# Kernel optimization log

Measured on AMD Instinct MI355X. Metric: run time of the kernel, lower is better.

## Reference

```python
import jax, jax.numpy as jnp
import numpy as np

E = 64        # num_experts
K = 6         # num_experts_per_tok
D = 2048      # hidden_size
F = 1408      # moe_intermediate_size (per expert)
NSH = 2       # num_shared_experts
FS = F * NSH  # shared-expert intermediate
T = 2048      # tokens (batch*seq flattened)
CAP = 512     # expert capacity; mean load T*K/E=192, CAP is >20 sigma above -> no drops


def setup_inputs() -> dict:
    key = jax.random.key(0)
    ks = jax.random.split(key, 9)
    s = 0.02
    return {
        "hidden_states": jax.random.normal(ks[0], (T, D), jnp.float32),
        "gate_w": jax.random.normal(ks[1], (E, D), jnp.float32) * s,
        "w_gate": jax.random.normal(ks[2], (E, D, F), jnp.float32) * s,
        "w_up": jax.random.normal(ks[3], (E, D, F), jnp.float32) * s,
        "w_down": jax.random.normal(ks[4], (E, F, D), jnp.float32) * s,
        "ws_gate": jax.random.normal(ks[5], (D, FS), jnp.float32) * s,
        "ws_up": jax.random.normal(ks[6], (D, FS), jnp.float32) * s,
        "ws_down": jax.random.normal(ks[7], (FS, D), jnp.float32) * s,
    }


def reference(hidden_states, gate_w, w_gate, w_up, w_down, ws_gate, ws_up, ws_down):
    x = hidden_states  # [T, D]
    n_tok = x.shape[0]

    # ---- gate: softmax -> top-k -> renormalize (bailing_moe norm_topk_prob) ----
    probs = jax.nn.softmax(x @ gate_w.T, axis=-1)           # [T, E]
    topw, topi = jax.lax.top_k(probs, K)                    # [T, K]
    topw = topw / jnp.sum(topw, axis=-1, keepdims=True)

    flat_e = topi.reshape(-1)                               # [T*K] expert id per assignment
    flat_w = topw.reshape(-1)                               # [T*K] combine weight
    tok = jnp.arange(n_tok * K) // K                        # [T*K] source token (idxs // k)

    # ---- dispatch: slot of each assignment within its expert (== sort-by-expert) ----
    onehot = jax.nn.one_hot(flat_e, E, dtype=jnp.int32)     # [T*K, E]
    slot = jnp.take_along_axis(jnp.cumsum(onehot, axis=0) - onehot,
                               flat_e[:, None], axis=1)[:, 0]  # [T*K]
    valid = slot < CAP                                      # all True given CAP margin
    slot_c = jnp.where(valid, slot, CAP - 1)

    xa = x[tok] * valid[:, None].astype(x.dtype)            # [T*K, D] gathered tokens
    buf = jnp.zeros((E, CAP, D), x.dtype).at[flat_e, slot_c].add(xa)  # [E, CAP, D]

    # ---- per-expert SwiGLU MLP as grouped GEMMs ----
    h = jax.nn.silu(jnp.einsum('ecd,edf->ecf', buf, w_gate)) \
        * jnp.einsum('ecd,edf->ecf', buf, w_up)             # [E, CAP, F]
    o = jnp.einsum('ecf,efd->ecd', h, w_down)               # [E, CAP, D]

    # ---- combine: weighted scatter-add back to tokens ----
    ya = o[flat_e, slot_c] * (flat_w * valid.astype(flat_w.dtype))[:, None]
    y = jax.ops.segment_sum(ya, tok, num_segments=n_tok)    # [T, D]

    # ---- shared experts (SwiGLU on identity) ----
    shared = (jax.nn.silu(x @ ws_gate) * (x @ ws_up)) @ ws_down
    return y + shared
```

## Files before the change

### kernel.cpp

```cpp
#include <hip/hip_runtime.h>
#include <hip/hip_bf16.h>
#include <cstdint>

typedef __attribute__((ext_vector_type(4))) float f4;
typedef __attribute__((ext_vector_type(4))) float f32x4;
typedef __attribute__((ext_vector_type(8))) __bf16 bf16x8;
typedef unsigned short ushort_t;
typedef unsigned int uint_t;

#define TTOK 2048
#define DDIM 2048
#define NEXP 64
#define TOPK 6
#define FDIM 1408
#define FSH  2816
#define NASSIGN (TTOK*TOPK)

__device__ __forceinline__ ushort_t f2bf(float f){
  uint_t u = __builtin_bit_cast(uint_t, f);
  u = (u + 0x7FFFu + ((u >> 16) & 1u)) >> 16;
  return (ushort_t)u;
}
__device__ __forceinline__ float bf2f(uint_t b){
  uint_t u = (b & 0xFFFFu) << 16;
  return __builtin_bit_cast(float, u);
}
__device__ __forceinline__ void gld_lds16(const void* g, void* l){
  __builtin_amdgcn_global_load_lds((const __attribute__((address_space(1))) uint_t*)g,
                                   (__attribute__((address_space(3))) uint_t*)l, 16, 0, 0);
}

__global__ __launch_bounds__(256) void gate_topk_kernel(
    const float* __restrict__ x, const float* __restrict__ gw,
    int* __restrict__ topi, float* __restrict__ topw)
{
  __shared__ float xs[4*2048];
  __shared__ float lg[4*64];
  int tid = threadIdx.x;
  int t0 = blockIdx.x*4;
  const f4* xg = (const f4*)(x + (size_t)t0*DDIM);
  f4* xsv = (f4*)xs;
  for (int i = tid; i < 2048; i += 256) xsv[i] = xg[i];
  __syncthreads();
  int g = tid >> 6, l = tid & 63;
  int c = l & 3, er = l >> 2;
  const f4* xrow = (const f4*)(xs + g*2048 + c*512);
  #pragma unroll
  for (int eo = 0; eo < 4; ++eo){
    int e = eo*16 + er;
    const f4* wrow = (const f4*)(gw + (size_t)e*DDIM + c*512);
    float d = 0.f;
    #pragma unroll 4
    for (int j = 0; j < 128; ++j){
      f4 w = wrow[j], a = xrow[j];
      d += w.x*a.x + w.y*a.y + w.z*a.z + w.w*a.w;
    }
    d += __shfl_xor(d, 1);
    d += __shfl_xor(d, 2);
    if (c == 0) lg[g*64 + e] = d;
  }
  __syncthreads();
  float mv = lg[g*64 + l];
  float sv[6]; int si[6];
  #pragma unroll
  for (int s = 0; s < 6; ++s){
    float bv = mv; int bi = l;
    for (int off = 32; off > 0; off >>= 1){
      float ov = __shfl_xor(bv, off);
      int oi = __shfl_xor(bi, off);
      if (ov > bv || (ov == bv && oi < bi)){ bv = ov; bi = oi; }
    }
    sv[s] = bv; si[s] = bi;
    if (l == bi) mv = -3.4e38f;
  }
  if (l == 0){
    float sum = 0.f, wv[6];
    #pragma unroll
    for (int s = 0; s < 6; ++s){ wv[s] = __expf(sv[s] - sv[0]); sum += wv[s]; }
    float inv = 1.f/sum;
    int t = t0 + g;
    #pragma unroll
    for (int s = 0; s < 6; ++s){ topi[t*6+s] = si[s]; topw[t*6+s] = wv[s]*inv; }
  }
}

__global__ __launch_bounds__(256) void xcast_kernel(const float* __restrict__ x, ushort_t* __restrict__ xb){
  size_t base = ((size_t)blockIdx.x*256 + threadIdx.x)*8;
  f4 a = *(const f4*)(x + base);
  f4 b = *(const f4*)(x + base + 4);
  uint4 r;
  r.x = f2bf(a.x) | ((uint_t)f2bf(a.y)<<16);
  r.y = f2bf(a.z) | ((uint_t)f2bf(a.w)<<16);
  r.z = f2bf(b.x) | ((uint_t)f2bf(b.y)<<16);
  r.w = f2bf(b.z) | ((uint_t)f2bf(b.w)<<16);
  *(uint4*)(xb + base) = r;
}

__global__ __launch_bounds__(256) void count_kernel(const int* __restrict__ topi, int* __restrict__ counts){
  int a = blockIdx.x*256 + threadIdx.x;
  if (a < NASSIGN) atomicAdd(&counts[topi[a]], 1);
}
__global__ void scan_kernel(const int* __restrict__ counts, int* __restrict__ offsets){
  if (threadIdx.x == 0){
    int s = 0;
    for (int e = 0; e < NEXP; ++e){ offsets[e] = s; s += counts[e]; }
    offsets[NEXP] = s;
  }
}
__global__ __launch_bounds__(256) void scatter_kernel(
    const int* __restrict__ topi, const float* __restrict__ topw,
    const int* __restrict__ offsets, int* __restrict__ cursor,
    int* __restrict__ row_token, float* __restrict__ row_w, int* __restrict__ row_assign)
{
  int a = blockIdx.x*256 + threadIdx.x;
  if (a < NASSIGN){
    int e = topi[a];
    int pos = atomicAdd(&cursor[e], 1);
    int r = offsets[e] + pos;
    row_token[r]  = a / 6;
    row_w[r]      = topw[a];
    row_assign[r] = a;
  }
}

__global__ __launch_bounds__(512, 2) void gemm_gateup_kernel(
    const ushort_t* __restrict__ A, const float* __restrict__ Bg0, const float* __restrict__ Bu0,
    ushort_t* __restrict__ H,
    const int* __restrict__ offsets, const int* __restrict__ row_token,
    const ushort_t* __restrict__ zerop,
    int N, int K, int lda, int n_mt, int n_nt, int Mfix)
{
  int nwg = gridDim.x;
  int chunk = nwg >> 3;
  int L = (blockIdx.x & 7)*chunk + (blockIdx.x >> 3);
  int e, mt, nt, row0, rowcnt;
  if (offsets){
    int per = n_mt*n_nt; e = L/per; int rem = L - e*per; mt = rem/n_nt; nt = rem - mt*n_nt;
    row0 = offsets[e]; rowcnt = offsets[e+1] - row0;
  } else { e = 0; nt = L/n_mt; mt = L - nt*n_mt; row0 = 0; rowcnt = Mfix; }
  int m0 = mt*256;
  if (m0 >= rowcnt) return;

  const float* Bg = Bg0 + (size_t)e*K*N + nt*64;
  const float* Bu = Bu0 + (size_t)e*K*N + nt*64;

  __shared__ ushort_t As[2][256*64];
  __shared__ ushort_t Bs[2][2*64*64];

  int tid = threadIdx.x;
  int lane = tid & 63;
  int wid = tid >> 6;
  int wm = wid & 3, wn = wid >> 2;

  const ushort_t* asrc[4];
  #pragma unroll
  for (int i = 0; i < 4; ++i){
    int r = (tid >> 3) + i*64;
    int gr = m0 + r;
    bool v = gr < rowcnt;
    int tok = row_token ? (v ? row_token[row0+gr] : 0) : gr;
    const ushort_t* p = v ? (A + (size_t)tok*lda) : zerop;
    int slot = (tid & 7) ^ (r & 7);
    asrc[i] = p + slot*8;
  }

  int half = tid >> 8;
  int l256 = tid & 255;
  int bn4 = l256 & 15, bk4 = l256 >> 4;
  const float* Bsrc = half ? Bu : Bg;
  int bdoff[4];
  #pragma unroll
  for (int j = 0; j < 4; ++j){
    int n = bn4*4 + j;
    int slot = (bk4 >> 1) ^ (n & 7);
    bdoff[j] = half*4096 + n*64 + slot*8 + (bk4 & 1)*4;
  }

  f32x4 accG[4][2], accU[4][2];
  #pragma unroll
  for (int i=0;i<4;++i)
    #pragma unroll
    for (int j=0;j<2;++j){ accG[i][j] = f32x4{0.f,0.f,0.f,0.f}; accU[i][j] = f32x4{0.f,0.f,0.f,0.f}; }

  int nK = K >> 6;
  #pragma unroll
  for (int i = 0; i < 4; ++i)
    gld_lds16(asrc[i], &As[0][i*4096 + tid*8]);
  {
    const float* bp = Bsrc + (size_t)(bk4*4)*N + bn4*4;
    f4 v0 = *(const f4*)(bp);
    f4 v1 = *(const f4*)(bp + (size_t)N);
    f4 v2 = *(const f4*)(bp + 2*(size_t)N);
    f4 v3 = *(const f4*)(bp + 3*(size_t)N);
    #pragma unroll
    for (int j = 0; j < 4; ++j){
      uint2 pk;
      pk.x = f2bf(v0[j]) | ((uint_t)f2bf(v1[j]) << 16);
      pk.y = f2bf(v2[j]) | ((uint_t)f2bf(v3[j]) << 16);
      *(uint2*)&Bs[0][bdoff[j]] = pk;
    }
  }
  __syncthreads();

  for (int ks = 0; ks < nK; ++ks){
    int cur = ks & 1, nxt = cur ^ 1;
    bool pf = (ks + 1) < nK;
    if (pf){
      int k0n = (ks + 1) << 6;
      #pragma unroll
      for (int i = 0; i < 4; ++i)
        gld_lds16(asrc[i] + k0n, &As[nxt][i*4096 + tid*8]);
    }
    f4 v0, v1, v2, v3;
    if (pf){
      const float* bp = Bsrc + (size_t)(((ks + 1) << 6) + bk4*4)*N + bn4*4;
      v0 = *(const f4*)(bp);
      v1 = *(const f4*)(bp + (size_t)N);
      v2 = *(const f4*)(bp + 2*(size_t)N);
      v3 = *(const f4*)(bp + 3*(size_t)N);
    }
    #pragma unroll
    for (int kk = 0; kk < 2; ++kk){
      bf16x8 af[4], bg[2], bu[2];
      int kb = (kk << 2) + (lane >> 4);
      #pragma unroll
      for (int i = 0; i < 4; ++i){
        int ar = wm*64 + i*16 + (lane & 15);
        af[i] = *(const bf16x8*)&As[cur][ar*64 + ((kb ^ (ar & 7)) << 3)];
      }
      #pragma unroll
      for (int j = 0; j < 2; ++j){
        int br = wn*32 + j*16 + (lane & 15);
        int idx = br*64 + ((kb ^ (br & 7)) << 3);
        bg[j] = *(const bf16x8*)&Bs[cur][idx];
        bu[j] = *(const bf16x8*)&Bs[cur][4096 + idx];
      }
      #pragma unroll
      for (int i = 0; i < 4; ++i)
        #pragma unroll
        for (int j = 0; j < 2; ++j){
          accG[i][j] = __builtin_amdgcn_mfma_f32_16x16x32_bf16(af[i], bg[j], accG[i][j], 0,0,0);
          accU[i][j] = __builtin_amdgcn_mfma_f32_16x16x32_bf16(af[i], bu[j], accU[i][j], 0,0,0);
        }
    }
    if (pf){
      #pragma unroll
      for (int j = 0; j < 4; ++j){
        uint2 pk;
        pk.x = f2bf(v0[j]) | ((uint_t)f2bf(v1[j]) << 16);
        pk.y = f2bf(v2[j]) | ((uint_t)f2bf(v3[j]) << 16);
        *(uint2*)&Bs[nxt][bdoff[j]] = pk;
      }
    }
    __syncthreads();
  }

  #pragma unroll
  for (int i = 0; i < 4; ++i)
    #pragma unroll
    for (int j = 0; j < 2; ++j){
      int col = nt*64 + wn*32 + j*16 + (lane & 15);
      #pragma unroll
      for (int q = 0; q < 4; ++q){
        int r = wm*64 + i*16 + ((lane >> 4) << 2) + q;
        int gr = m0 + r;
        if (gr < rowcnt){
          float gv = accG[i][j][q];
          float uv = accU[i][j][q];
          float hv = (gv / (1.f + __expf(-gv))) * uv;
          H[(size_t)(row0 + gr)*(size_t)N + col] = f2bf(hv);
        }
      }
    }
}

__global__ __launch_bounds__(512, 4) void gemm_down_kernel(
    const ushort_t* __restrict__ A, const float* __restrict__ B0,
    ushort_t* __restrict__ outb, float* __restrict__ outf,
    const int* __restrict__ offsets, const float* __restrict__ row_w, const int* __restrict__ row_assign,
    const ushort_t* __restrict__ zerop,
    int N, int K, int lda, int n_mt, int n_nt, int Mfix)
{
  int nwg = gridDim.x;
  int chunk = nwg >> 3;
  int L = (blockIdx.x & 7)*chunk + (blockIdx.x >> 3);
  int e, mt, nt, row0, rowcnt;
  if (offsets){
    int per = n_mt*n_nt; e = L/per; int rem = L - e*per; mt = rem/n_nt; nt = rem - mt*n_nt;
    row0 = offsets[e]; rowcnt = offsets[e+1] - row0;
  } else { e = 0; nt = L/n_mt; mt = L - nt*n_mt; row0 = 0; rowcnt = Mfix; }
  int m0 = mt*256;
  if (m0 >= rowcnt) return;

  const float* B = B0 + (size_t)e*K*N + nt*64;

  __shared__ ushort_t As[2][256*64];
  __shared__ ushort_t Bs[2][64*64];
  __shared__ float Wr[256];
  __shared__ int Ar[256];

  int tid = threadIdx.x;
  int lane = tid & 63;
  int wid = tid >> 6;
  int wm = wid & 3, wn = wid >> 2;

  if (offsets){
    for (int t = tid; t < 256; t += 512){
      int gr = m0 + t;
      bool v = gr < rowcnt;
      Wr[t] = v ? row_w[row0+gr] : 0.f;
      Ar[t] = v ? row_assign[row0+gr] : 0;
    }
  }

  const ushort_t* asrc[4];
  #pragma unroll
  for (int i = 0; i < 4; ++i){
    int r = (tid >> 3) + i*64;
    int gr = m0 + r;
    bool v = gr < rowcnt;
    const ushort_t* p = v ? (A + (size_t)(row0+gr)*lda) : zerop;
    int slot = (tid & 7) ^ (r & 7);
    asrc[i] = p + slot*8;
  }

  int bn4 = tid & 15, bk8 = tid >> 4;
  int bdoff[4];
  #pragma unroll
  for (int j = 0; j < 4; ++j){
    int n = bn4*4 + j;
    int slot = (bk8 >> 2) ^ (n & 7);
    bdoff[j] = n*64 + slot*8 + (bk8 & 3)*2;
  }

  f32x4 acc[4][2];
  #pragma unroll
  for (int i=0;i<4;++i)
    #pragma unroll
    for (int j=0;j<2;++j) acc[i][j] = f32x4{0.f,0.f,0.f,0.f};

  int nK = K >> 6;
  #pragma unroll
  for (int i = 0; i < 4; ++i)
    gld_lds16(asrc[i], &As[0][i*4096 + tid*8]);
  {
    const float* bp = B + (size_t)(bk8*2)*N + bn4*4;
    f4 v0 = *(const f4*)(bp);
    f4 v1 = *(const f4*)(bp + (size_t)N);
    #pragma unroll
    for (int j = 0; j < 4; ++j){
      uint_t pk = f2bf(v0[j]) | ((uint_t)f2bf(v1[j]) << 16);
      *(uint_t*)&Bs[0][bdoff[j]] = pk;
    }
  }
  __syncthreads();

  for (int ks = 0; ks < nK; ++ks){
    int cur = ks & 1, nxt = cur ^ 1;
    bool pf = (ks + 1) < nK;
    if (pf){
      int k0n = (ks + 1) << 6;
      #pragma unroll
      for (int i = 0; i < 4; ++i)
        gld_lds16(asrc[i] + k0n, &As[nxt][i*4096 + tid*8]);
    }
    f4 v0, v1;
    if (pf){
      const float* bp = B + (size_t)(((ks + 1) << 6) + bk8*2)*N + bn4*4;
      v0 = *(const f4*)(bp);
      v1 = *(const f4*)(bp + (size_t)N);
    }
    #pragma unroll
    for (int kk = 0; kk < 2; ++kk){
      bf16x8 af[4], bb[2];
      int kb = (kk << 2) + (lane >> 4);
      #pragma unroll
      for (int i = 0; i < 4; ++i){
        int ar = wm*64 + i*16 + (lane & 15);
        af[i] = *(const bf16x8*)&As[cur][ar*64 + ((kb ^ (ar & 7)) << 3)];
      }
      #pragma unroll
      for (int j = 0; j < 2; ++j){
        int br = wn*32 + j*16 + (lane & 15);
        bb[j] = *(const bf16x8*)&Bs[cur][br*64 + ((kb ^ (br & 7)) << 3)];
      }
      #pragma unroll
      for (int i = 0; i < 4; ++i)
        #pragma unroll
        for (int j = 0; j < 2; ++j)
          acc[i][j] = __builtin_amdgcn_mfma_f32_16x16x32_bf16(af[i], bb[j], acc[i][j], 0,0,0);
    }
    if (pf){
      #pragma unroll
      for (int j = 0; j < 4; ++j){
        uint_t pk = f2bf(v0[j]) | ((uint_t)f2bf(v1[j]) << 16);
        *(uint_t*)&Bs[nxt][bdoff[j]] = pk;
      }
    }
    __syncthreads();
  }

  #pragma unroll
  for (int i = 0; i < 4; ++i)
    #pragma unroll
    for (int j = 0; j < 2; ++j){
      int col = nt*64 + wn*32 + j*16 + (lane & 15);
      #pragma unroll
      for (int q = 0; q < 4; ++q){
        int r = wm*64 + i*16 + ((lane >> 4) << 2) + q;
        int gr = m0 + r;
        if (gr < rowcnt){
          float val = acc[i][j][q];
          if (offsets){
            outb[(size_t)Ar[r]*2048 + col] = f2bf(val * Wr[r]);
          } else {
            outf[(size_t)gr*2048 + col] = val;
          }
        }
      }
    }
}

__global__ __launch_bounds__(256) void combine_kernel(const ushort_t* __restrict__ oa, float* __restrict__ out){
  size_t base = ((size_t)blockIdx.x*256 + threadIdx.x)*8;
  int t = (int)(base >> 11);
  int d = (int)(base & 2047);
  f4 s0 = *(const f4*)(out + base);
  f4 s1 = *(const f4*)(out + base + 4);
  #pragma unroll
  for (int k = 0; k < 6; ++k){
    const ushort_t* row = oa + (((size_t)(t*6+k)) << 11) + d;
    uint4 u = *(const uint4*)row;
    s0.x += bf2f(u.x); s0.y += bf2f(u.x >> 16);
    s0.z += bf2f(u.y); s0.w += bf2f(u.y >> 16);
    s1.x += bf2f(u.z); s1.y += bf2f(u.z >> 16);
    s1.z += bf2f(u.w); s1.w += bf2f(u.w >> 16);
  }
  *(f4*)(out + base) = s0;
  *(f4*)(out + base + 4) = s1;
}

extern "C" void kernel_launch(void* const* d_in, const int* in_sizes, int n_in,
                              void* d_out, int out_size, void* d_ws, size_t ws_size,
                              hipStream_t stream)
{
  const float* x       = (const float*)d_in[0];
  const float* gate_w  = (const float*)d_in[1];
  const float* w_gate  = (const float*)d_in[2];
  const float* w_up    = (const float*)d_in[3];
  const float* w_down  = (const float*)d_in[4];
  const float* ws_gate = (const float*)d_in[5];
  const float* ws_up   = (const float*)d_in[6];
  const float* ws_down = (const float*)d_in[7];
  float* out = (float*)d_out;

  char* ws = (char*)d_ws;
  int*      topi       = (int*)(ws + 0);
  float*    topw       = (float*)(ws + 49152);
  int*      counts     = (int*)(ws + 98304);
  int*      cursor     = (int*)(ws + 98560);
  int*      offsets    = (int*)(ws + 98816);
  int*      row_token  = (int*)(ws + 99328);
  float*    row_w      = (float*)(ws + 148480);
  int*      row_assign = (int*)(ws + 197632);
  ushort_t* zerop      = (ushort_t*)(ws + 262144);
  ushort_t* xb         = (ushort_t*)(ws + 524288);
  ushort_t* Hbuf       = (ushort_t*)(ws + 8912896);
  ushort_t* Shbuf      = (ushort_t*)(ws + 43515904);
  ushort_t* oa         = (ushort_t*)(ws + 55050240);
  (void)ws_size; (void)in_sizes; (void)n_in; (void)out_size;

  hipMemsetAsync(ws + 98304, 0, 512, stream);
  hipMemsetAsync(zerop, 0, 8192, stream);

  gate_topk_kernel<<<512, 256, 0, stream>>>(x, gate_w, topi, topw);
  xcast_kernel<<<2048, 256, 0, stream>>>(x, xb);
  count_kernel<<<48, 256, 0, stream>>>(topi, counts);
  scan_kernel<<<1, 64, 0, stream>>>(counts, offsets);
  scatter_kernel<<<48, 256, 0, stream>>>(topi, topw, offsets, cursor, row_token, row_w, row_assign);

  gemm_gateup_kernel<<<2816, 512, 0, stream>>>(xb, w_gate, w_up, Hbuf, offsets, row_token, zerop,
                                               FDIM, DDIM, DDIM, 2, 22, 0);
  gemm_gateup_kernel<<<352, 512, 0, stream>>>(xb, ws_gate, ws_up, Shbuf, nullptr, nullptr, zerop,
                                              FSH, DDIM, DDIM, 8, 44, TTOK);
  gemm_down_kernel<<<256, 512, 0, stream>>>(Shbuf, ws_down, nullptr, out, nullptr, nullptr, nullptr, zerop,
                                            DDIM, FSH, FSH, 8, 32, TTOK);
  gemm_down_kernel<<<4096, 512, 0, stream>>>(Hbuf, w_down, oa, nullptr, offsets, row_w, row_assign, zerop,
                                             DDIM, FDIM, FDIM, 2, 32, 0);
  combine_kernel<<<2048, 256, 0, stream>>>(oa, out);
}
```

Measured before the change: 1.135 ms.

## Single-buffer B tile, hand-tune waitcnt/barriers, and re-swizzle LDS in grouped GEMMs

Both grouped GEMM kernels now keep the bf16-converted B tile in a single LDS buffer instead of a double buffer. __syncthreads is replaced with explicit s_waitcnt vmcnt/lgkmcnt plus raw s_barrier, so the async A loads to LDS can stay in flight while compute runs. The A/B LDS swizzle gains an extra XOR with row bits 3-5 to reduce bank conflicts, and gate/up launch bounds go from 2 to 4 blocks per CU for higher occupancy. The risks are register spills under the tighter bound and correctness hazards from the hand-counted vmcnt values and the raw barriers. The LDS savings are also probably too small to actually fit 4 blocks.

Result: slower. 1.280 ms (+12.8%).

```diff
diff --git a/kernel.cpp b/kernel.cpp
--- a/kernel.cpp
+++ b/kernel.cpp
@@ -15,6 +15,10 @@
 #define FDIM 1408
 #define FSH  2816
 #define NASSIGN (TTOK*TOPK)
+
+#define SBAR()     __asm__ __volatile__("s_barrier" ::: "memory")
+#define WAITVMC(N) __asm__ __volatile__("s_waitcnt vmcnt(" #N ")" ::: "memory")
+#define WAITLG()   __asm__ __volatile__("s_waitcnt lgkmcnt(0)" ::: "memory")
 
 __device__ __forceinline__ ushort_t f2bf(float f){
   uint_t u = __builtin_bit_cast(uint_t, f);
@@ -123,7 +127,7 @@
   }
 }
 
-__global__ __launch_bounds__(512, 2) void gemm_gateup_kernel(
+__global__ __launch_bounds__(512, 4) void gemm_gateup_kernel(
     const ushort_t* __restrict__ A, const float* __restrict__ Bg0, const float* __restrict__ Bu0,
     ushort_t* __restrict__ H,
     const int* __restrict__ offsets, const int* __restrict__ row_token,
@@ -145,13 +149,14 @@
   const float* Bu = Bu0 + (size_t)e*K*N + nt*64;
 
   __shared__ ushort_t As[2][256*64];
-  __shared__ ushort_t Bs[2][2*64*64];
+  __shared__ ushort_t Bsh[2*64*64];
 
   int tid = threadIdx.x;
   int lane = tid & 63;
   int wid = tid >> 6;
   int wm = wid & 3, wn = wid >> 2;
 
+  int aslot = (tid & 7) ^ ((tid >> 3) & 7) ^ ((tid >> 6) & 7);
   const ushort_t* asrc[4];
   #pragma unroll
   for (int i = 0; i < 4; ++i){
@@ -160,8 +165,7 @@
     bool v = gr < rowcnt;
     int tok = row_token ? (v ? row_token[row0+gr] : 0) : gr;
     const ushort_t* p = v ? (A + (size_t)tok*lda) : zerop;
-    int slot = (tid & 7) ^ (r & 7);
-    asrc[i] = p + slot*8;
+    asrc[i] = p + aslot*8;
   }
 
   int half = tid >> 8;
@@ -172,8 +176,8 @@
   #pragma unroll
   for (int j = 0; j < 4; ++j){
     int n = bn4*4 + j;
-    int slot = (bk4 >> 1) ^ (n & 7);
-    bdoff[j] = half*4096 + n*64 + slot*8 + (bk4 & 1)*4;
+    int pchunk = ((bk4 >> 1) ^ (n & 7) ^ ((n >> 3) & 7)) & 7;
+    bdoff[j] = half*4096 + n*64 + pchunk*8 + (bk4 & 1)*4;
   }
 
   f32x4 accG[4][2], accU[4][2];
@@ -183,9 +187,6 @@
     for (int j=0;j<2;++j){ accG[i][j] = f32x4{0.f,0.f,0.f,0.f}; accU[i][j] = f32x4{0.f,0.f,0.f,0.f}; }
 
   int nK = K >> 6;
-  #pragma unroll
-  for (int i = 0; i < 4; ++i)
-    gld_lds16(asrc[i], &As[0][i*4096 + tid*8]);
   {
     const float* bp = Bsrc + (size_t)(bk4*4)*N + bn4*4;
     f4 v0 = *(const f4*)(bp);
@@ -193,24 +194,21 @@
     f4 v2 = *(const f4*)(bp + 2*(size_t)N);
     f4 v3 = *(const f4*)(bp + 3*(size_t)N);
     #pragma unroll
+    for (int i = 0; i < 4; ++i)
+      gld_lds16(asrc[i], &As[0][i*4096 + tid*8]);
+    #pragma unroll
     for (int j = 0; j < 4; ++j){
       uint2 pk;
       pk.x = f2bf(v0[j]) | ((uint_t)f2bf(v1[j]) << 16);
       pk.y = f2bf(v2[j]) | ((uint_t)f2bf(v3[j]) << 16);
-      *(uint2*)&Bs[0][bdoff[j]] = pk;
-    }
-  }
-  __syncthreads();
+      *(uint2*)&Bsh[bdoff[j]] = pk;
+    }
+    WAITLG();
+  }
 
   for (int ks = 0; ks < nK; ++ks){
     int cur = ks & 1, nxt = cur ^ 1;
     bool pf = (ks + 1) < nK;
-    if (pf){
-      int k0n = (ks + 1) << 6;
-      #pragma unroll
-      for (int i = 0; i < 4; ++i)
-        gld_lds16(asrc[i] + k0n, &As[nxt][i*4096 + tid*8]);
-    }
     f4 v0, v1, v2, v3;
     if (pf){
       const float* bp = Bsrc + (size_t)(((ks + 1) << 6) + bk4*4)*N + bn4*4;
@@ -218,7 +216,16 @@
       v1 = *(const f4*)(bp + (size_t)N);
       v2 = *(const f4*)(bp + 2*(size_t)N);
       v3 = *(const f4*)(bp + 3*(size_t)N);
-    }
+      int k0n = (ks + 1) << 6;
+      #pragma unroll
+      for (int i = 0; i < 4; ++i)
+        gld_lds16(asrc[i] + k0n, &As[nxt][i*4096 + tid*8]);
+      WAITVMC(8);
+    } else {
+      WAITVMC(0);
+    }
+    SBAR();
+
     #pragma unroll
     for (int kk = 0; kk < 2; ++kk){
       bf16x8 af[4], bg[2], bu[2];
@@ -226,14 +233,15 @@
       #pragma unroll
       for (int i = 0; i < 4; ++i){
         int ar = wm*64 + i*16 + (lane & 15);
-        af[i] = *(const bf16x8*)&As[cur][ar*64 + ((kb ^ (ar & 7)) << 3)];
+        int ch = (kb ^ (ar & 7) ^ ((ar >> 3) & 7)) & 7;
+        af[i] = *(const bf16x8*)&As[cur][ar*64 + (ch << 3)];
       }
       #pragma unroll
       for (int j = 0; j < 2; ++j){
         int br = wn*32 + j*16 + (lane & 15);
-        int idx = br*64 + ((kb ^ (br & 7)) << 3);
-        bg[j] = *(const bf16x8*)&Bs[cur][idx];
-        bu[j] = *(const bf16x8*)&Bs[cur][4096 + idx];
+        int ch = (kb ^ (br & 7) ^ ((br >> 3) & 7)) & 7;
+        bg[j] = *(const bf16x8*)&Bsh[br*64 + (ch << 3)];
+        bu[j] = *(const bf16x8*)&Bsh[4096 + br*64 + (ch << 3)];
       }
       #pragma unroll
       for (int i = 0; i < 4; ++i)
@@ -243,16 +251,17 @@
           accU[i][j] = __builtin_amdgcn_mfma_f32_16x16x32_bf16(af[i], bu[j], accU[i][j], 0,0,0);
         }
     }
+    SBAR();
     if (pf){
       #pragma unroll
       for (int j = 0; j < 4; ++j){
         uint2 pk;
         pk.x = f2bf(v0[j]) | ((uint_t)f2bf(v1[j]) << 16);
         pk.y = f2bf(v2[j]) | ((uint_t)f2bf(v3[j]) << 16);
-        *(uint2*)&Bs[nxt][bdoff[j]] = pk;
-      }
-    }
-    __syncthreads();
+        *(uint2*)&Bsh[bdoff[j]] = pk;
+      }
+      WAITLG();
+    }
   }
 
   #pragma unroll
@@ -295,7 +304,7 @@
   const float* B = B0 + (size_t)e*K*N + nt*64;
 
   __shared__ ushort_t As[2][256*64];
-  __shared__ ushort_t Bs[2][64*64];
+  __shared__ ushort_t Bs[64*64];
   __shared__ float Wr[256];
   __shared__ int Ar[256];
 
@@ -313,6 +322,7 @@
     }
   }
 
+  int aslot = (tid & 7) ^ ((tid >> 3) & 7) ^ ((tid >> 6) & 7);
   const ushort_t* asrc[4];
   #pragma unroll
   for (int i = 0; i < 4; ++i){
@@ -320,8 +330,7 @@
     int gr = m0 + r;
     bool v = gr < rowcnt;
     const ushort_t* p = v ? (A + (size_t)(row0+gr)*lda) : zerop;
-    int slot = (tid & 7) ^ (r & 7);
-    asrc[i] = p + slot*8;
+    asrc[i] = p + aslot*8;
   }
 
   int bn4 = tid & 15, bk8 = tid >> 4;
@@ -329,8 +338,8 @@
   #pragma unroll
   for (int j = 0; j < 4; ++j){
     int n = bn4*4 + j;
-    int slot = (bk8 >> 2) ^ (n & 7);
-    bdoff[j] = n*64 + slot*8 + (bk8 & 3)*2;
+    int pchunk = ((bk8 >> 2) ^ (n & 7) ^ ((n >> 3) & 7)) & 7;
+    bdoff[j] = n*64 + pchunk*8 + (bk8 & 3)*2;
   }
 
   f32x4 acc[4][2];
@@ -340,36 +349,39 @@
     for (int j=0;j<2;++j) acc[i][j] = f32x4{0.f,0.f,0.f,0.f};
 
   int nK = K >> 6;
-  #pragma unroll
-  for (int i = 0; i < 4; ++i)
-    gld_lds16(asrc[i], &As[0][i*4096 + tid*8]);
   {
     const float* bp = B + (size_t)(bk8*2)*N + bn4*4;
     f4 v0 = *(const f4*)(bp);
     f4 v1 = *(const f4*)(bp + (size_t)N);
     #pragma unroll
+    for (int i = 0; i < 4; ++i)
+      gld_lds16(asrc[i], &As[0][i*4096 + tid*8]);
+    #pragma unroll
     for (int j = 0; j < 4; ++j){
       uint_t pk = f2bf(v0[j]) | ((uint_t)f2bf(v1[j]) << 16);
-      *(uint_t*)&Bs[0][bdoff[j]] = pk;
-    }
-  }
-  __syncthreads();
+      *(uint_t*)&Bs[bdoff[j]] = pk;
+    }
+    WAITLG();
+  }
 
   for (int ks = 0; ks < nK; ++ks){
     int cur = ks & 1, nxt = cur ^ 1;
     bool pf = (ks + 1) < nK;
-    if (pf){
-      int k0n = (ks + 1) << 6;
-      #pragma unroll
-      for (int i = 0; i < 4; ++i)
-        gld_lds16(asrc[i] + k0n, &As[nxt][i*4096 + tid*8]);
-    }
     f4 v0, v1;
     if (pf){
       const float* bp = B + (size_t)(((ks + 1) << 6) + bk8*2)*N + bn4*4;
       v0 = *(const f4*)(bp);
       v1 = *(const f4*)(bp + (size_t)N);
-    }
+      int k0n = (ks + 1) << 6;
+      #pragma unroll
+      for (int i = 0; i < 4; ++i)
+        gld_lds16(asrc[i] + k0n, &As[nxt][i*4096 + tid*8]);
+      WAITVMC(6);
+    } else {
+      WAITVMC(0);
+    }
+    SBAR();
+
     #pragma unroll
     for (int kk = 0; kk < 2; ++kk){
       bf16x8 af[4], bb[2];
@@ -377,12 +389,14 @@
       #pragma unroll
       for (int i = 0; i < 4; ++i){
         int ar = wm*64 + i*16 + (lane & 15);
-        af[i] = *(const bf16x8*)&As[cur][ar*64 + ((kb ^ (ar & 7)) << 3)];
+        int ch = (kb ^ (ar & 7) ^ ((ar >> 3) & 7)) & 7;
+        af[i] = *(const bf16x8*)&As[cur][ar*64 + (ch << 3)];
       }
       #pragma unroll
       for (int j = 0; j < 2; ++j){
         int br = wn*32 + j*16 + (lane & 15);
-        bb[j] = *(const bf16x8*)&Bs[cur][br*64 + ((kb ^ (br & 7)) << 3)];
+        int ch = (kb ^ (br & 7) ^ ((br >> 3) & 7)) & 7;
+        bb[j] = *(const bf16x8*)&Bs[br*64 + (ch << 3)];
       }
       #pragma unroll
       for (int i = 0; i < 4; ++i)
@@ -390,14 +404,15 @@
         for (int j = 0; j < 2; ++j)
           acc[i][j] = __builtin_amdgcn_mfma_f32_16x16x32_bf16(af[i], bb[j], acc[i][j], 0,0,0);
     }
+    SBAR();
     if (pf){
       #pragma unroll
       for (int j = 0; j < 4; ++j){
         uint_t pk = f2bf(v0[j]) | ((uint_t)f2bf(v1[j]) << 16);
-        *(uint_t*)&Bs[nxt][bdoff[j]] = pk;
-      }
-    }
-    __syncthreads();
+        *(uint_t*)&Bs[bdoff[j]] = pk;
+      }
+      WAITLG();
+    }
   }
 
   #pragma unroll
```
